# Optimization experiments

Hardware: AMD Instinct MI355X
Metric: run time of the kernel (lower is better)

The kernel has to match this reference:

```python
import jax, jax.numpy as jnp
import numpy as np

NUM_HEADS = 16
HEAD_DIM = 128  # hidden_size 2048 / 16 heads


def setup_inputs() -> dict:
    key = jax.random.key(0)
    k1, k2, k3 = jax.random.split(key, 3)
    bsz, seq, hidden = 2, 2048, 2048
    return {
        "query": jax.random.normal(k1, (bsz, seq, hidden), dtype=jnp.float32),
        "key": jax.random.normal(k2, (bsz, seq, hidden), dtype=jnp.float32),
        "value": jax.random.normal(k3, (bsz, seq, hidden), dtype=jnp.float32),
        "attention_mask": jnp.zeros((1, 1, seq, seq), dtype=jnp.float32),
    }


def reference(query, key, value, attention_mask):
    bsz, seq, hidden = query.shape
    h, d = NUM_HEADS, HEAD_DIM
    # (b, s, h*d) -> (b, h, s, d)
    q = query.reshape(bsz, seq, h, d).transpose(0, 2, 1, 3)
    k = key.reshape(bsz, seq, h, d).transpose(0, 2, 1, 3)
    v = value.reshape(bsz, seq, h, d).transpose(0, 2, 1, 3)
    # scores: (b, h, s, s)
    scores = jnp.einsum("bhqd,bhkd->bhqk", q, k) / jnp.sqrt(jnp.float32(d))
    scores = scores + attention_mask
    probs = jax.nn.softmax(scores.astype(jnp.float32), axis=-1).astype(q.dtype)
    out = jnp.einsum("bhqk,bhkd->bhqd", probs, v)
    # (b, h, s, d) -> (b, s, h*d)
    return out.transpose(0, 2, 1, 3).reshape(bsz, seq, hidden)
```

## Files before the change

kernel.cpp:

```cpp
#include <hip/hip_runtime.h>
#include <hip/hip_bf16.h>
#include <math.h>

#define SEQ 2048
#define NH 16
#define HD 128
#define HID 2048
#define KVB 64
#define NKT (SEQ/KVB)
#define QB 128
#define QBLK 64

typedef __attribute__((ext_vector_type(8))) short bf16x8;
typedef __attribute__((ext_vector_type(4))) short bf16x4;
typedef __attribute__((ext_vector_type(4))) float f32x4;

#define SCL2E 0.1275310261f
#define L2E   1.4426950408889634f

__device__ __forceinline__ short f2bf(float x){
  __hip_bfloat16 h = __float2bfloat16(x);
  return *reinterpret_cast<short*>(&h);
}

__device__ __forceinline__ void gld_lds16(const void* g, void* l){
  __builtin_amdgcn_global_load_lds((const __attribute__((address_space(1))) void*)g,
                                   (__attribute__((address_space(3))) void*)l, 16, 0, 0);
}

__global__ void zero_flag_k(int* f){ if (threadIdx.x == 0) *f = 0; }

__global__ void mask_scan_k(const float* __restrict__ m, int n4, int* __restrict__ flag){
  int any = 0;
  const float4* m4 = (const float4*)m;
  for (int i = blockIdx.x*blockDim.x + threadIdx.x; i < n4; i += gridDim.x*blockDim.x){
    float4 v = m4[i];
    any |= (v.x != 0.f) | (v.y != 0.f) | (v.z != 0.f) | (v.w != 0.f);
  }
  if (__ballot(any) != 0ull && (threadIdx.x & 63) == 0) atomicOr(flag, 1);
}

__global__ void cvt_qk_k(const float* __restrict__ in, short* __restrict__ out){
  const int n4 = (2*SEQ*HID)/4;
  for (int i = blockIdx.x*blockDim.x + threadIdx.x; i < n4; i += gridDim.x*blockDim.x){
    int i4 = i*4;
    int b   = i4 >> 22;
    int rem = i4 & ((1<<22)-1);
    int s   = rem >> 11;
    int hd  = rem & 2047;
    int h = hd >> 7, d = hd & 127;
    float4 v = *(const float4*)(in + i4);
    bf16x4 o; o[0]=f2bf(v.x); o[1]=f2bf(v.y); o[2]=f2bf(v.z); o[3]=f2bf(v.w);
    *(bf16x4*)(out + ((size_t)((b*NH + h)*SEQ + s))*HD + d) = o;
  }
}

__global__ void cvt_vt_k(const float* __restrict__ Vg, short* __restrict__ Vt){
  __shared__ short T[64*HD];
  const int bh = blockIdx.x >> 5, st = blockIdx.x & 31;
  const int b = bh >> 4, h = bh & 15;
  const int s0 = st*64;
  const int tid = threadIdx.x;
  const float* vp = Vg + ((size_t)(b*SEQ + s0))*HID + h*HD;
  #pragma unroll
  for (int i = 0; i < 8; ++i){
    int idx = tid + i*256;
    int r = idx >> 5, c4 = idx & 31;
    float4 v = *(const float4*)(vp + (size_t)r*HID + c4*4);
    int X = ((r & 7) ^ ((r >> 3) & 7)) << 3;
    bf16x4 o; o[0]=f2bf(v.x); o[1]=f2bf(v.y); o[2]=f2bf(v.z); o[3]=f2bf(v.w);
    *(bf16x4*)(&T[r*HD + ((c4*4) ^ X)]) = o;
  }
  __syncthreads();
  short* op = Vt + ((size_t)bh*HD)*SEQ + s0;
  #pragma unroll
  for (int u = 0; u < 4; ++u){
    int unit = tid + u*256;
    int sb = unit & 7, d = unit >> 3;
    bf16x8 pk;
    #pragma unroll
    for (int j = 0; j < 8; ++j)
      pk[j] = T[(sb*8 + j)*HD + (d ^ (((j ^ sb) & 7) << 3))];
    *(bf16x8*)(op + (size_t)d*SEQ + sb*8) = pk;
  }
}

__launch_bounds__(256, 2)
__global__ void attn_bf_k(const short* __restrict__ Qb, const short* __restrict__ Kb,
                          const short* __restrict__ Vtb, const float* __restrict__ Mg,
                          float* __restrict__ Og, const int* __restrict__ flagp)
{
  __shared__ __align__(16) short Kl[2][KVB*HD];
  __shared__ __align__(16) short Vl[2][HD*KVB];
  __shared__ __align__(16) short Pl[4][32*KVB];

  const int tid = threadIdx.x;
  const int w = tid >> 6, lane = tid & 63;
  const int lo = lane & 15, hi = lane >> 4;
  const int swz = (lo & 7) << 3;

  int bid = blockIdx.x;
  bid = (bid & 7)*64 + (bid >> 3);
  const int bh = bid >> 4;
  const int qt = bid & 15;
  const int b = bh >> 4, h = bh & 15;
  const int mflag = *flagp;

  bf16x8 qfA[4], qfB[4];
  {
    const short* qa = Qb + ((size_t)bh*SEQ + qt*QB + w*32 + lo)*HD;
    const short* qb2 = qa + 16*HD;
    #pragma unroll
    for (int kc = 0; kc < 4; ++kc){
      qfA[kc] = *(const bf16x8*)(qa + kc*32 + hi*8);
      qfB[kc] = *(const bf16x8*)(qb2 + kc*32 + hi*8);
    }
  }

  const short* kbase = Kb + (size_t)bh*SEQ*HD;
  const short* vbase = Vtb + (size_t)bh*HD*SEQ;
  int koff[4], voff[4], cdst[4];
  #pragma unroll
  for (int c = 0; c < 4; ++c){
    int p = (c*4 + w)*1024 + lane*16;
    cdst[c] = (c*4 + w)*1024;
    int r  = p >> 8;
    int cs = (p & 255) >> 1;
    koff[c] = r*HD + (cs ^ ((r & 7) << 3));
    int d   = p >> 7;
    int cs2 = (p & 127) >> 1;
    voff[c] = d*SEQ + (cs2 ^ ((d & 7) << 3));
  }

  auto stage = [&](int bufi, int kt){
    const short* ks = kbase + kt*(KVB*HD);
    const short* vs = vbase + kt*KVB;
    char* kl = (char*)&Kl[bufi][0];
    char* vl = (char*)&Vl[bufi][0];
    #pragma unroll
    for (int c = 0; c < 4; ++c){
      gld_lds16(ks + koff[c], kl + cdst[c]);
      gld_lds16(vs + voff[c], vl + cdst[c]);
    }
  };

  f32x4 accA[8], accB[8];
  #pragma unroll
  for (int i = 0; i < 8; ++i){
    accA[i][0]=0.f; accA[i][1]=0.f; accA[i][2]=0.f; accA[i][3]=0.f;
    accB[i][0]=0.f; accB[i][1]=0.f; accB[i][2]=0.f; accB[i][3]=0.f;
  }
  float mA = -INFINITY, lA = 0.f, mB = -INFINITY, lB = 0.f;

  stage(0, 0);
  asm volatile("s_waitcnt vmcnt(0)" ::: "memory");
  __syncthreads();

  int buf = 0;
  for (int kt = 0; kt < NKT; ++kt){
    if (kt + 1 < NKT) stage(buf^1, kt+1);

    const short* Kc = &Kl[buf][0];
    const short* Vc = &Vl[buf][0];

    float pA[4][4], pB[4][4];
    #pragma unroll
    for (int nb = 0; nb < 4; ++nb){
      f32x4 sA = {0.f,0.f,0.f,0.f}, sB = {0.f,0.f,0.f,0.f};
      const int krow = nb*16 + lo;
      #pragma unroll
      for (int kc = 0; kc < 4; ++kc){
        bf16x8 kf = *(const bf16x8*)(Kc + ((krow*HD + kc*32 + hi*8) ^ swz));
        sA = __builtin_amdgcn_mfma_f32_16x16x32_bf16(kf, qfA[kc], sA, 0, 0, 0);
        sB = __builtin_amdgcn_mfma_f32_16x16x32_bf16(kf, qfB[kc], sB, 0, 0, 0);
      }
      if (mflag){
        const float* mr  = Mg + (size_t)(qt*QB + w*32 + lo)*SEQ + kt*KVB + nb*16 + hi*4;
        const float* mr2 = mr + (size_t)16*SEQ;
        #pragma unroll
        for (int r = 0; r < 4; ++r){
          pA[nb][r] = sA[r]*SCL2E + mr[r]*L2E;
          pB[nb][r] = sB[r]*SCL2E + mr2[r]*L2E;
        }
      } else {
        #pragma unroll
        for (int r = 0; r < 4; ++r){
          pA[nb][r] = sA[r]*SCL2E;
          pB[nb][r] = sB[r]*SCL2E;
        }
      }
    }

    auto online = [&](float (&p)[4][4], float& m, float& l, f32x4 (&acc)[8]){
      float pm = p[0][0];
      #pragma unroll
      for (int nb = 0; nb < 4; ++nb)
        #pragma unroll
        for (int r = 0; r < 4; ++r) pm = fmaxf(pm, p[nb][r]);
      pm = fmaxf(pm, __shfl_xor(pm, 16, 64));
      pm = fmaxf(pm, __shfl_xor(pm, 32, 64));
      float mn = fmaxf(m, pm);
      if (!__all(pm - m <= 8.0f)){
        float fac = exp2f(m - mn);
        m = mn; l *= fac;
        #pragma unroll
        for (int r2 = 0; r2 < 4; ++r2){
          float fr = __shfl(fac, hi*4 + r2, 64);
          #pragma unroll
          for (int oc = 0; oc < 8; ++oc) acc[oc][r2] *= fr;
        }
      }
      float rs = 0.f;
      #pragma unroll
      for (int nb = 0; nb < 4; ++nb)
        #pragma unroll
        for (int r = 0; r < 4; ++r){
          float e = exp2f(p[nb][r] - m);
          p[nb][r] = e; rs += e;
        }
      rs += __shfl_xor(rs, 16, 64);
      rs += __shfl_xor(rs, 32, 64);
      l += rs;
    };
    online(pA, mA, lA, accA);
    online(pB, mB, lB, accB);

    short* myP = &Pl[w][0];
    #pragma unroll
    for (int nb = 0; nb < 4; ++nb){
      bf16x4 ka, kb2;
      #pragma unroll
      for (int r = 0; r < 4; ++r){ ka[r] = f2bf(pA[nb][r]); kb2[r] = f2bf(pB[nb][r]); }
      *(bf16x4*)(myP + ((lo*KVB + nb*16 + hi*4) ^ swz)) = ka;
      *(bf16x4*)(myP + (((16+lo)*KVB + nb*16 + hi*4) ^ swz)) = kb2;
    }

    #pragma unroll
    for (int kc2 = 0; kc2 < 2; ++kc2){
      bf16x8 paA = *(const bf16x8*)(myP + ((lo*KVB + kc2*32 + hi*8) ^ swz));
      bf16x8 paB = *(const bf16x8*)(myP + (((16+lo)*KVB + kc2*32 + hi*8) ^ swz));
      #pragma unroll
      for (int oc = 0; oc < 8; ++oc){
        int vr = oc*16 + lo;
        bf16x8 vf = *(const bf16x8*)(Vc + ((vr*KVB + kc2*32 + hi*8) ^ swz));
        accA[oc] = __builtin_amdgcn_mfma_f32_16x16x32_bf16(paA, vf, accA[oc], 0, 0, 0);
        accB[oc] = __builtin_amdgcn_mfma_f32_16x16x32_bf16(paB, vf, accB[oc], 0, 0, 0);
      }
    }

    asm volatile("s_waitcnt vmcnt(0)" ::: "memory");
    __syncthreads();
    buf ^= 1;
  }

  float* obase = Og + ((size_t)(b*SEQ + qt*QB + w*32))*HID + h*HD;
  #pragma unroll
  for (int r = 0; r < 4; ++r){
    float liA = 1.0f / __shfl(lA, hi*4 + r, 64);
    float liB = 1.0f / __shfl(lB, hi*4 + r, 64);
    #pragma unroll
    for (int oc = 0; oc < 8; ++oc){
      obase[(size_t)(hi*4 + r)*HID + oc*16 + lo]      = accA[oc][r]*liA;
      obase[(size_t)(16 + hi*4 + r)*HID + oc*16 + lo] = accB[oc][r]*liB;
    }
  }
}

__launch_bounds__(256)
__global__ void attn_f32_k(const float* __restrict__ Qg, const float* __restrict__ Kg,
                           const float* __restrict__ Vg, const float* __restrict__ Mg,
                           float* __restrict__ Og, const int* __restrict__ flagp)
{
  __shared__ __align__(16) short Kl[KVB*HD];
  __shared__ __align__(16) short Vt[HD*KVB];
  __shared__ __align__(16) short Pl[4][16*KVB];

  const int tid  = threadIdx.x;
  const int w    = tid >> 6;
  const int lane = tid & 63;
  const int lo   = lane & 15;
  const int hi   = lane >> 4;

  int bid = blockIdx.x;
  bid = (bid & 7)*128 + (bid >> 3);
  const int bh = bid >> 5;
  const int qt = bid & 31;
  const int b  = bh >> 4;
  const int h  = bh & 15;
  const int mflag = *flagp;

  bf16x8 qf[4];
  {
    const float* qrow = Qg + ((size_t)(b*SEQ + qt*QBLK + w*16 + lo))*HID + h*HD;
    #pragma unroll
    for (int kc = 0; kc < 4; ++kc){
      float4 v0 = *(const float4*)(qrow + kc*32 + hi*8);
      float4 v1 = *(const float4*)(qrow + kc*32 + hi*8 + 4);
      bf16x8 q;
      q[0]=f2bf(v0.x); q[1]=f2bf(v0.y); q[2]=f2bf(v0.z); q[3]=f2bf(v0.w);
      q[4]=f2bf(v1.x); q[5]=f2bf(v1.y); q[6]=f2bf(v1.z); q[7]=f2bf(v1.w);
      qf[kc] = q;
    }
  }

  f32x4 acc[8];
  #pragma unroll
  for (int i = 0; i < 8; ++i){ acc[i][0]=0.f; acc[i][1]=0.f; acc[i][2]=0.f; acc[i][3]=0.f; }
  float mrow[4] = {-INFINITY, -INFINITY, -INFINITY, -INFINITY};
  float lrow[4] = {0.f, 0.f, 0.f, 0.f};

  const float* kb = Kg + ((size_t)b*SEQ)*HID + h*HD;
  const float* vb = Vg + ((size_t)b*SEQ)*HID + h*HD;

  for (int kt = 0; kt < NKT; ++kt){
    __syncthreads();
    {
      const float* kp = kb + (size_t)(kt*KVB)*HID;
      #pragma unroll
      for (int i = 0; i < 8; ++i){
        int idx = tid + i*256;
        int r  = idx >> 5;
        int c4 = idx & 31;
        float4 v = *(const float4*)(kp + (size_t)r*HID + c4*4);
        int sidx = (r*HD + c4*4) ^ ((r & 7) << 3);
        short* dst = &Kl[sidx];
        dst[0]=f2bf(v.x); dst[1]=f2bf(v.y); dst[2]=f2bf(v.z); dst[3]=f2bf(v.w);
      }
      const float* vp = vb + (size_t)(kt*KVB)*HID;
      #pragma unroll
      for (int u = 0; u < 4; ++u){
        int unit = tid + u*256;
        int d   = unit & 127;
        int g   = unit >> 7;
        int kv0 = g*8;
        bf16x8 pk;
        #pragma unroll
        for (int j = 0; j < 8; ++j)
          pk[j] = f2bf(vp[(size_t)(kv0 + j)*HID + d]);
        int sidx = (d*KVB + kv0) ^ ((d & 7) << 3);
        *(bf16x8*)(&Vt[sidx]) = pk;
      }
    }
    __syncthreads();

    f32x4 sv[4];
    #pragma unroll
    for (int nb = 0; nb < 4; ++nb){ sv[nb][0]=0.f; sv[nb][1]=0.f; sv[nb][2]=0.f; sv[nb][3]=0.f; }
    #pragma unroll
    for (int nb = 0; nb < 4; ++nb){
      int krow = nb*16 + lo;
      #pragma unroll
      for (int kc = 0; kc < 4; ++kc){
        int sidx = (krow*HD + kc*32 + hi*8) ^ ((krow & 7) << 3);
        bf16x8 kf = *(const bf16x8*)(&Kl[sidx]);
        sv[nb] = __builtin_amdgcn_mfma_f32_16x16x32_bf16(qf[kc], kf, sv[nb], 0, 0, 0);
      }
    }

    float p[4][4];
    if (mflag){
      #pragma unroll
      for (int nb = 0; nb < 4; ++nb)
        #pragma unroll
        for (int r = 0; r < 4; ++r){
          float mv = Mg[(size_t)(qt*QBLK + w*16 + hi*4 + r)*SEQ + kt*KVB + nb*16 + lo];
          p[nb][r] = sv[nb][r]*SCL2E + mv*L2E;
        }
    } else {
      #pragma unroll
      for (int nb = 0; nb < 4; ++nb)
        #pragma unroll
        for (int r = 0; r < 4; ++r)
          p[nb][r] = sv[nb][r]*SCL2E;
    }

    #pragma unroll
    for (int r = 0; r < 4; ++r){
      float mx = fmaxf(fmaxf(p[0][r], p[1][r]), fmaxf(p[2][r], p[3][r]));
      mx = fmaxf(mx, __shfl_xor(mx, 1, 64));
      mx = fmaxf(mx, __shfl_xor(mx, 2, 64));
      mx = fmaxf(mx, __shfl_xor(mx, 4, 64));
      mx = fmaxf(mx, __shfl_xor(mx, 8, 64));
      float mn  = fmaxf(mrow[r], mx);
      float fac = exp2f(mrow[r] - mn);
      mrow[r] = mn;
      lrow[r] *= fac;
      #pragma unroll
      for (int oc = 0; oc < 8; ++oc) acc[oc][r] *= fac;
      float rs = 0.f;
      #pragma unroll
      for (int nb = 0; nb < 4; ++nb){
        float e = exp2f(p[nb][r] - mn);
        p[nb][r] = e;
        rs += e;
      }
      rs += __shfl_xor(rs, 1, 64);
      rs += __shfl_xor(rs, 2, 64);
      rs += __shfl_xor(rs, 4, 64);
      rs += __shfl_xor(rs, 8, 64);
      lrow[r] += rs;
    }

    short* myP = &Pl[w][0];
    #pragma unroll
    for (int nb = 0; nb < 4; ++nb)
      #pragma unroll
      for (int r = 0; r < 4; ++r){
        int row = hi*4 + r;
        int sidx = (row*KVB + nb*16 + lo) ^ ((row & 7) << 3);
        myP[sidx] = f2bf(p[nb][r]);
      }

    #pragma unroll
    for (int kc2 = 0; kc2 < 2; ++kc2){
      int sA = (lo*KVB + kc2*32 + hi*8) ^ ((lo & 7) << 3);
      bf16x8 pa = *(const bf16x8*)(&myP[sA]);
      #pragma unroll
      for (int oc = 0; oc < 8; ++oc){
        int vrow = oc*16 + lo;
        int sB = (vrow*KVB + kc2*32 + hi*8) ^ ((vrow & 7) << 3);
        bf16x8 vf = *(const bf16x8*)(&Vt[sB]);
        acc[oc] = __builtin_amdgcn_mfma_f32_16x16x32_bf16(pa, vf, acc[oc], 0, 0, 0);
      }
    }
  }

  float* orow = Og + ((size_t)(b*SEQ + qt*QBLK + w*16))*HID + h*HD;
  #pragma unroll
  for (int r = 0; r < 4; ++r){
    float inv = 1.0f / lrow[r];
    #pragma unroll
    for (int oc = 0; oc < 8; ++oc)
      orow[(size_t)(hi*4 + r)*HID + oc*16 + lo] = acc[oc][r]*inv;
  }
}

extern "C" void kernel_launch(void* const* d_in, const int* in_sizes, int n_in,
                              void* d_out, int out_size, void* d_ws, size_t ws_size,
                              hipStream_t stream)
{
  const float* Qg = (const float*)d_in[0];
  const float* Kg = (const float*)d_in[1];
  const float* Vg = (const float*)d_in[2];
  const float* Mg = (const float*)d_in[3];
  float* Og = (float*)d_out;
  int* flag = (int*)d_ws;

  const size_t plane = (size_t)2*NH*SEQ*HD;
  const size_t need = 64 + 3*plane*sizeof(short);

  hipLaunchKernelGGL(zero_flag_k, dim3(1), dim3(1), 0, stream, flag);
  hipLaunchKernelGGL(mask_scan_k, dim3(256), dim3(256), 0, stream, Mg, SEQ*SEQ/4, flag);

  if (ws_size >= need){
    short* Qb = (short*)((char*)d_ws + 64);
    short* Kb = Qb + plane;
    short* Vt = Kb + plane;
    hipLaunchKernelGGL(cvt_qk_k, dim3(2048), dim3(256), 0, stream, Qg, Qb);
    hipLaunchKernelGGL(cvt_qk_k, dim3(2048), dim3(256), 0, stream, Kg, Kb);
    hipLaunchKernelGGL(cvt_vt_k, dim3(1024), dim3(256), 0, stream, Vg, Vt);
    hipLaunchKernelGGL(attn_bf_k, dim3(512), dim3(256), 0, stream, Qb, Kb, Vt, Mg, Og, flag);
  } else {
    hipLaunchKernelGGL(attn_f32_k, dim3(32*32), dim3(256), 0, stream, Qg, Kg, Vg, Mg, Og, flag);
  }
}
```

Baseline: 146.9 us.

## Switch attention to 32x32x16 MFMA with in-register P via permlane swap

Rewrites the main attention kernel to use 32x32x16 bf16 MFMA tiles, one 32-row query tile per wave. The softmax probabilities are packed with v_cvt_pk_bf16_f32 and rearranged with permlane32_swap instead of a round trip through LDS, which removes the P shared buffer. Q is now read directly from fp32 and converted inside the kernel, dropping the separate Q conversion kernel and its workspace. s_setprio is raised around the MFMA blocks, and the flag-zeroing kernel becomes a memset. The larger tiles raise register pressure (4 f32x16 accumulators plus 32 probabilities per lane), which may hurt occupancy.

```diff
diff --git a/kernel.cpp b/kernel.cpp
--- a/kernel.cpp
+++ b/kernel.cpp
@@ -14,6 +14,8 @@
 typedef __attribute__((ext_vector_type(8))) short bf16x8;
 typedef __attribute__((ext_vector_type(4))) short bf16x4;
 typedef __attribute__((ext_vector_type(4))) float f32x4;
+typedef __attribute__((ext_vector_type(16))) float f32x16;
+typedef __attribute__((ext_vector_type(2))) unsigned uint2v;
 
 #define SCL2E 0.1275310261f
 #define L2E   1.4426950408889634f
@@ -23,12 +25,16 @@
   return *reinterpret_cast<short*>(&h);
 }
 
+__device__ __forceinline__ unsigned cvtpk(float lo, float hi){
+  unsigned r;
+  asm("v_cvt_pk_bf16_f32 %0, %1, %2" : "=v"(r) : "v"(lo), "v"(hi));
+  return r;
+}
+
 __device__ __forceinline__ void gld_lds16(const void* g, void* l){
   __builtin_amdgcn_global_load_lds((const __attribute__((address_space(1))) void*)g,
                                    (__attribute__((address_space(3))) void*)l, 16, 0, 0);
 }
-
-__global__ void zero_flag_k(int* f){ if (threadIdx.x == 0) *f = 0; }
 
 __global__ void mask_scan_k(const float* __restrict__ m, int n4, int* __restrict__ flag){
   int any = 0;
@@ -86,18 +92,17 @@
 }
 
 __launch_bounds__(256, 2)
-__global__ void attn_bf_k(const short* __restrict__ Qb, const short* __restrict__ Kb,
-                          const short* __restrict__ Vtb, const float* __restrict__ Mg,
-                          float* __restrict__ Og, const int* __restrict__ flagp)
+__global__ void attn32_k(const float* __restrict__ Qg, const short* __restrict__ Kb,
+                         const short* __restrict__ Vtb, const float* __restrict__ Mg,
+                         float* __restrict__ Og, const int* __restrict__ flagp)
 {
   __shared__ __align__(16) short Kl[2][KVB*HD];
   __shared__ __align__(16) short Vl[2][HD*KVB];
-  __shared__ __align__(16) short Pl[4][32*KVB];
 
   const int tid = threadIdx.x;
   const int w = tid >> 6, lane = tid & 63;
-  const int lo = lane & 15, hi = lane >> 4;
-  const int swz = (lo & 7) << 3;
+  const int l31 = lane & 31, hi1 = lane >> 5;
+  const int swz = (lane & 7) << 3;
 
   int bid = blockIdx.x;
   bid = (bid & 7)*64 + (bid >> 3);
@@ -105,17 +110,7 @@
   const int qt = bid & 15;
   const int b = bh >> 4, h = bh & 15;
   const int mflag = *flagp;
-
-  bf16x8 qfA[4], qfB[4];
-  {
-    const short* qa = Qb + ((size_t)bh*SEQ + qt*QB + w*32 + lo)*HD;
-    const short* qb2 = qa + 16*HD;
-    #pragma unroll
-    for (int kc = 0; kc < 4; ++kc){
-      qfA[kc] = *(const bf16x8*)(qa + kc*32 + hi*8);
-      qfB[kc] = *(const bf16x8*)(qb2 + kc*32 + hi*8);
-    }
-  }
+  const int qrow_g = qt*QB + w*32 + l31;
 
   const short* kbase = Kb + (size_t)bh*SEQ*HD;
   const short* vbase = Vtb + (size_t)bh*HD*SEQ;
@@ -131,7 +126,6 @@
     int cs2 = (p & 127) >> 1;
     voff[c] = d*SEQ + (cs2 ^ ((d & 7) << 3));
   }
-
   auto stage = [&](int bufi, int kt){
     const short* ks = kbase + kt*(KVB*HD);
     const short* vs = vbase + kt*KVB;
@@ -144,15 +138,29 @@
     }
   };
 
-  f32x4 accA[8], accB[8];
-  #pragma unroll
-  for (int i = 0; i < 8; ++i){
-    accA[i][0]=0.f; accA[i][1]=0.f; accA[i][2]=0.f; accA[i][3]=0.f;
-    accB[i][0]=0.f; accB[i][1]=0.f; accB[i][2]=0.f; accB[i][3]=0.f;
-  }
-  float mA = -INFINITY, lA = 0.f, mB = -INFINITY, lB = 0.f;
-
   stage(0, 0);
+
+  bf16x8 qf[8];
+  {
+    const float* qrow = Qg + ((size_t)(b*SEQ + qrow_g))*HID + h*HD;
+    #pragma unroll
+    for (int ks = 0; ks < 8; ++ks){
+      float4 a = *(const float4*)(qrow + ks*16 + hi1*8);
+      float4 c = *(const float4*)(qrow + ks*16 + hi1*8 + 4);
+      bf16x8 q;
+      q[0]=f2bf(a.x); q[1]=f2bf(a.y); q[2]=f2bf(a.z); q[3]=f2bf(a.w);
+      q[4]=f2bf(c.x); q[5]=f2bf(c.y); q[6]=f2bf(c.z); q[7]=f2bf(c.w);
+      qf[ks] = q;
+    }
+  }
+
+  f32x16 acc[4];
+  #pragma unroll
+  for (int cb = 0; cb < 4; ++cb)
+    #pragma unroll
+    for (int i = 0; i < 16; ++i) acc[cb][i] = 0.f;
+  float m_ = -INFINITY, l_ = 0.f;
+
   asm volatile("s_waitcnt vmcnt(0)" ::: "memory");
   __syncthreads();
 
@@ -163,107 +171,103 @@
     const short* Kc = &Kl[buf][0];
     const short* Vc = &Vl[buf][0];
 
-    float pA[4][4], pB[4][4];
-    #pragma unroll
-    for (int nb = 0; nb < 4; ++nb){
-      f32x4 sA = {0.f,0.f,0.f,0.f}, sB = {0.f,0.f,0.f,0.f};
-      const int krow = nb*16 + lo;
-      #pragma unroll
-      for (int kc = 0; kc < 4; ++kc){
-        bf16x8 kf = *(const bf16x8*)(Kc + ((krow*HD + kc*32 + hi*8) ^ swz));
-        sA = __builtin_amdgcn_mfma_f32_16x16x32_bf16(kf, qfA[kc], sA, 0, 0, 0);
-        sB = __builtin_amdgcn_mfma_f32_16x16x32_bf16(kf, qfB[kc], sB, 0, 0, 0);
-      }
-      if (mflag){
-        const float* mr  = Mg + (size_t)(qt*QB + w*32 + lo)*SEQ + kt*KVB + nb*16 + hi*4;
-        const float* mr2 = mr + (size_t)16*SEQ;
+    f32x16 sv0, sv1;
+    #pragma unroll
+    for (int i = 0; i < 16; ++i){ sv0[i] = 0.f; sv1[i] = 0.f; }
+    const short* krow0 = Kc + l31*HD;
+    __builtin_amdgcn_s_setprio(1);
+    #pragma unroll
+    for (int ks = 0; ks < 8; ++ks){
+      int o = (ks*16 + hi1*8) ^ swz;
+      bf16x8 kf0 = *(const bf16x8*)(krow0 + o);
+      bf16x8 kf1 = *(const bf16x8*)(krow0 + 32*HD + o);
+      sv0 = __builtin_amdgcn_mfma_f32_32x32x16_bf16(kf0, qf[ks], sv0, 0, 0, 0);
+      sv1 = __builtin_amdgcn_mfma_f32_32x32x16_bf16(kf1, qf[ks], sv1, 0, 0, 0);
+    }
+    __builtin_amdgcn_s_setprio(0);
+
+    float p[32];
+    if (mflag){
+      const float* mrow = Mg + (size_t)qrow_g*SEQ + kt*KVB;
+      #pragma unroll
+      for (int i = 0; i < 16; ++i){
+        int kv0 = (i&3) + 8*(i>>2) + 4*hi1;
+        p[i]    = sv0[i]*SCL2E + mrow[kv0]*L2E;
+        p[16+i] = sv1[i]*SCL2E + mrow[32+kv0]*L2E;
+      }
+    } else {
+      #pragma unroll
+      for (int i = 0; i < 16; ++i){ p[i] = sv0[i]*SCL2E; p[16+i] = sv1[i]*SCL2E; }
+    }
+
+    float pm = p[0];
+    #pragma unroll
+    for (int i = 1; i < 32; ++i) pm = fmaxf(pm, p[i]);
+    {
+      uint2v r = __builtin_amdgcn_permlane32_swap(__float_as_uint(pm), __float_as_uint(pm), false, false);
+      pm = fmaxf(__uint_as_float(r[0]), __uint_as_float(r[1]));
+    }
+    float mn = fmaxf(m_, pm);
+    if (!__all(pm - m_ <= 8.0f)){
+      float fac = exp2f(m_ - mn);
+      m_ = mn; l_ *= fac;
+      #pragma unroll
+      for (int cb = 0; cb < 4; ++cb)
         #pragma unroll
-        for (int r = 0; r < 4; ++r){
-          pA[nb][r] = sA[r]*SCL2E + mr[r]*L2E;
-          pB[nb][r] = sB[r]*SCL2E + mr2[r]*L2E;
-        }
-      } else {
-        #pragma unroll
-        for (int r = 0; r < 4; ++r){
-          pA[nb][r] = sA[r]*SCL2E;
-          pB[nb][r] = sB[r]*SCL2E;
-        }
-      }
-    }
-
-    auto online = [&](float (&p)[4][4], float& m, float& l, f32x4 (&acc)[8]){
-      float pm = p[0][0];
-      #pragma unroll
-      for (int nb = 0; nb < 4; ++nb)
-        #pragma unroll
-        for (int r = 0; r < 4; ++r) pm = fmaxf(pm, p[nb][r]);
-      pm = fmaxf(pm, __shfl_xor(pm, 16, 64));
-      pm = fmaxf(pm, __shfl_xor(pm, 32, 64));
-      float mn = fmaxf(m, pm);
-      if (!__all(pm - m <= 8.0f)){
-        float fac = exp2f(m - mn);
-        m = mn; l *= fac;
-        #pragma unroll
-        for (int r2 = 0; r2 < 4; ++r2){
-          float fr = __shfl(fac, hi*4 + r2, 64);
-          #pragma unroll
-          for (int oc = 0; oc < 8; ++oc) acc[oc][r2] *= fr;
-        }
-      }
-      float rs = 0.f;
-      #pragma unroll
-      for (int nb = 0; nb < 4; ++nb)
-        #pragma unroll
-        for (int r = 0; r < 4; ++r){
-          float e = exp2f(p[nb][r] - m);
-          p[nb][r] = e; rs += e;
-        }
-      rs += __shfl_xor(rs, 16, 64);
-      rs += __shfl_xor(rs, 32, 64);
-      l += rs;
-    };
-    online(pA, mA, lA, accA);
-    online(pB, mB, lB, accB);
-
-    short* myP = &Pl[w][0];
-    #pragma unroll
-    for (int nb = 0; nb < 4; ++nb){
-      bf16x4 ka, kb2;
-      #pragma unroll
-      for (int r = 0; r < 4; ++r){ ka[r] = f2bf(pA[nb][r]); kb2[r] = f2bf(pB[nb][r]); }
-      *(bf16x4*)(myP + ((lo*KVB + nb*16 + hi*4) ^ swz)) = ka;
-      *(bf16x4*)(myP + (((16+lo)*KVB + nb*16 + hi*4) ^ swz)) = kb2;
-    }
-
-    #pragma unroll
-    for (int kc2 = 0; kc2 < 2; ++kc2){
-      bf16x8 paA = *(const bf16x8*)(myP + ((lo*KVB + kc2*32 + hi*8) ^ swz));
-      bf16x8 paB = *(const bf16x8*)(myP + (((16+lo)*KVB + kc2*32 + hi*8) ^ swz));
-      #pragma unroll
-      for (int oc = 0; oc < 8; ++oc){
-        int vr = oc*16 + lo;
-        bf16x8 vf = *(const bf16x8*)(Vc + ((vr*KVB + kc2*32 + hi*8) ^ swz));
-        accA[oc] = __builtin_amdgcn_mfma_f32_16x16x32_bf16(paA, vf, accA[oc], 0, 0, 0);
-        accB[oc] = __builtin_amdgcn_mfma_f32_16x16x32_bf16(paB, vf, accB[oc], 0, 0, 0);
-      }
-    }
+        for (int i = 0; i < 16; ++i) acc[cb][i] *= fac;
+    }
+    float rs = 0.f;
+    #pragma unroll
+    for (int i = 0; i < 32; ++i){ float e = exp2f(p[i] - m_); p[i] = e; rs += e; }
+    {
+      uint2v r = __builtin_amdgcn_permlane32_swap(__float_as_uint(rs), __float_as_uint(rs), false, false);
+      rs = __uint_as_float(r[0]) + __uint_as_float(r[1]);
+    }
+    l_ += rs;
+
+    bf16x8 pa[4];
+    #pragma unroll
+    for (int sl = 0; sl < 4; ++sl){
+      const int ib = 8*(sl & 1) + 16*(sl >> 1);
+      unsigned A0 = cvtpk(p[ib+0], p[ib+1]);
+      unsigned A1 = cvtpk(p[ib+2], p[ib+3]);
+      unsigned B0 = cvtpk(p[ib+4], p[ib+5]);
+      unsigned B1 = cvtpk(p[ib+6], p[ib+7]);
+      uint2v r0 = __builtin_amdgcn_permlane32_swap(A0, B0, false, false);
+      uint2v r1 = __builtin_amdgcn_permlane32_swap(A1, B1, false, false);
+      union { unsigned u[4]; bf16x8 v; } t;
+      t.u[0] = r0[0]; t.u[1] = r1[0]; t.u[2] = r0[1]; t.u[3] = r1[1];
+      pa[sl] = t.v;
+    }
+
+    __builtin_amdgcn_s_setprio(1);
+    #pragma unroll
+    for (int sl = 0; sl < 4; ++sl){
+      int o = (sl*16 + hi1*8) ^ swz;
+      #pragma unroll
+      for (int cb = 0; cb < 4; ++cb){
+        bf16x8 vf = *(const bf16x8*)(Vc + (cb*32 + l31)*KVB + o);
+        acc[cb] = __builtin_amdgcn_mfma_f32_32x32x16_bf16(vf, pa[sl], acc[cb], 0, 0, 0);
+      }
+    }
+    __builtin_amdgcn_s_setprio(0);
 
     asm volatile("s_waitcnt vmcnt(0)" ::: "memory");
     __syncthreads();
     buf ^= 1;
   }
 
-  float* obase = Og + ((size_t)(b*SEQ + qt*QB + w*32))*HID + h*HD;
-  #pragma unroll
-  for (int r = 0; r < 4; ++r){
-    float liA = 1.0f / __shfl(lA, hi*4 + r, 64);
-    float liB = 1.0f / __shfl(lB, hi*4 + r, 64);
-    #pragma unroll
-    for (int oc = 0; oc < 8; ++oc){
-      obase[(size_t)(hi*4 + r)*HID + oc*16 + lo]      = accA[oc][r]*liA;
-      obase[(size_t)(16 + hi*4 + r)*HID + oc*16 + lo] = accB[oc][r]*liB;
-    }
-  }
+  float inv = 1.0f / l_;
+  float* orow = Og + ((size_t)(b*SEQ + qrow_g))*HID + h*HD;
+  #pragma unroll
+  for (int cb = 0; cb < 4; ++cb)
+    #pragma unroll
+    for (int g = 0; g < 4; ++g){
+      float4 o;
+      o.x = acc[cb][g*4+0]*inv; o.y = acc[cb][g*4+1]*inv;
+      o.z = acc[cb][g*4+2]*inv; o.w = acc[cb][g*4+3]*inv;
+      *(float4*)(orow + cb*32 + g*8 + 4*hi1) = o;
+    }
 }
 
 __launch_bounds__(256)
@@ -387,18 +391,18 @@
       lrow[r] *= fac;
       #pragma unroll
       for (int oc = 0; oc < 8; ++oc) acc[oc][r] *= fac;
-      float rs = 0.f;
+      float rsv = 0.f;
       #pragma unroll
       for (int nb = 0; nb < 4; ++nb){
         float e = exp2f(p[nb][r] - mn);
         p[nb][r] = e;
-        rs += e;
-      }
-      rs += __shfl_xor(rs, 1, 64);
-      rs += __shfl_xor(rs, 2, 64);
-      rs += __shfl_xor(rs, 4, 64);
-      rs += __shfl_xor(rs, 8, 64);
-      lrow[r] += rs;
+        rsv += e;
+      }
+      rsv += __shfl_xor(rsv, 1, 64);
+      rsv += __shfl_xor(rsv, 2, 64);
+      rsv += __shfl_xor(rsv, 4, 64);
+      rsv += __shfl_xor(rsv, 8, 64);
+      lrow[r] += rsv;
     }
 
     short* myP = &Pl[w][0];
@@ -447,19 +451,17 @@
   int* flag = (int*)d_ws;
 
   const size_t plane = (size_t)2*NH*SEQ*HD;
-  const size_t need = 64 + 3*plane*sizeof(short);
-
-  hipLaunchKernelGGL(zero_flag_k, dim3(1), dim3(1), 0, stream, flag);
+  const size_t need = 64 + 2*plane*sizeof(short);
+
+  hipMemsetAsync(d_ws, 0, 4, stream);
   hipLaunchKernelGGL(mask_scan_k, dim3(256), dim3(256), 0, stream, Mg, SEQ*SEQ/4, flag);
 
   if (ws_size >= need){
-    short* Qb = (short*)((char*)d_ws + 64);
-    short* Kb = Qb + plane;
+    short* Kb = (short*)((char*)d_ws + 64);
     short* Vt = Kb + plane;
-    hipLaunchKernelGGL(cvt_qk_k, dim3(2048), dim3(256), 0, stream, Qg, Qb);
     hipLaunchKernelGGL(cvt_qk_k, dim3(2048), dim3(256), 0, stream, Kg, Kb);
     hipLaunchKernelGGL(cvt_vt_k, dim3(1024), dim3(256), 0, stream, Vg, Vt);
-    hipLaunchKernelGGL(attn_bf_k, dim3(512), dim3(256), 0, stream, Qb, Kb, Vt, Mg, Og, flag);
+    hipLaunchKernelGGL(attn32_k, dim3(512), dim3(256), 0, stream, Qg, Kb, Vt, Mg, Og, flag);
   } else {
     hipLaunchKernelGGL(attn_f32_k, dim3(32*32), dim3(256), 0, stream, Qg, Kg, Vg, Mg, Og, flag);
   }
```

After: 134.5 us. 1.09x faster.
